# Optimization experiments

Measured on AMD Instinct MI355X. Metric: run time of the kernel, lower is better.

Reference implementation:

```python
import jax, jax.numpy as jnp
import numpy as np

N = 50000
E = 1600000
INPUT_DIM = 128
HEADS = 4
OUT_DIM = 32
LRELU_ALPHA = 0.2


def setup_inputs() -> dict:
    key = jax.random.key(0)
    k1, k2, k3, k4, k5 = jax.random.split(key, 5)
    gain = 1.0 / (1.0 + LRELU_ALPHA)
    input_proj = jax.random.normal(k1, (N, INPUT_DIM), dtype=jnp.float32)
    edge_index = jax.random.randint(k2, (2, E), 0, N, dtype=jnp.int64)
    W = jax.random.normal(k3, (INPUT_DIM, HEADS * OUT_DIM), dtype=jnp.float32) * (gain / INPUT_DIM) ** 0.5
    A_left = jax.random.normal(k4, (HEADS, OUT_DIM, 1), dtype=jnp.float32) * (gain / OUT_DIM)
    A_right = jax.random.normal(k5, (HEADS, OUT_DIM, 1), dtype=jnp.float32) * (gain / OUT_DIM)
    return {"input_proj": input_proj, "edge_index": edge_index, "W": W, "A_left": A_left, "A_right": A_right}


def reference(input_proj, edge_index, W, A_left, A_right):
    n = input_proj.shape[0]
    heads, out_dim = A_left.shape[0], A_left.shape[1]
    # Linear projection: [N, heads, out_dim]
    H = (input_proj @ W).reshape(n, heads, out_dim)
    # Per-node attention scores: [N, heads]
    H_s = jnp.einsum('nhd,hd->nh', H, A_left[..., 0])
    H_t = jnp.einsum('nhd,hd->nh', H, A_right[..., 0])
    src = edge_index[0]
    tgt = edge_index[1]
    # Edge scores: leaky_relu(H_s[src] + H_t[tgt]) -> [E, heads]
    e = H_s[src] + H_t[tgt]
    e = jnp.where(e > 0, e, LRELU_ALPHA * e)
    # Segment softmax over neighborhoods keyed by source node (global max shift, as in original)
    e = jnp.exp(e - jnp.max(e))
    denom = jax.ops.segment_sum(e, src, num_segments=n)  # [N, heads]
    alpha = e / (denom[src] + 1e-8)
    # Weighted scatter-add aggregation of target features: [N, heads, out_dim]
    msg = alpha[:, :, None] * H[tgt]
    agg = jax.ops.segment_sum(msg, src, num_segments=n)
    # concat_last=True -> [N, heads*out_dim], then ELU
    res = agg.reshape(n, heads * out_dim)
    return jax.nn.elu(res)
```

## Files before the change

kernel.cpp:

```cpp
#include <hip/hip_runtime.h>

#define DIM 128
#define HEADS 4
#define ODIM 32
#define LRELU 0.2f
#define PT 4096
#define CAP 9216

typedef unsigned int u32;
typedef unsigned short u16;
typedef unsigned char u8;

typedef __attribute__((ext_vector_type(8))) short bf16x8;
typedef __attribute__((ext_vector_type(4))) float f32x4;

__device__ __forceinline__ u16 f2bf(float f) {
    union { u32 u; float f; } x; x.f = f;
    u32 u = x.u;
    u32 r = u + 0x7FFFu + ((u >> 16) & 1u);
    return (u16)(r >> 16);
}
__device__ __forceinline__ float blo(u32 b) {
    union { u32 u; float f; } x; x.u = b << 16; return x.f;
}
__device__ __forceinline__ float bhi(u32 b) {
    union { u32 u; float f; } x; x.u = b & 0xFFFF0000u; return x.f;
}

__device__ __forceinline__ int scan256_excl(int v, int t, int* wsum) {
    int lane = t & 63, w = t >> 6;
    int inc = v;
    #pragma unroll
    for (int ofs = 1; ofs < 64; ofs <<= 1) {
        int x = __shfl_up(inc, ofs);
        if (lane >= ofs) inc += x;
    }
    __syncthreads();
    if (lane == 63) wsum[w] = inc;
    __syncthreads();
    int add = 0;
    #pragma unroll
    for (int j = 0; j < 4; ++j) add += (j < w) ? wsum[j] : 0;
    return inc - v + add;
}

__global__ __launch_bounds__(256) void prep_kernel(
    const float* __restrict__ W, u16* __restrict__ Wt, int* __restrict__ bcur)
{
    __shared__ u16 s[128 * 17];
    const int t = threadIdx.x;
    const int b = blockIdx.x;
    if (b == 0) bcur[t] = t * CAP;
    #pragma unroll
    for (int i = 0; i < 8; ++i) {
        int idx = i * 256 + t;
        int kk = idx >> 7;
        int nn = idx & 127;
        s[nn * 17 + kk] = f2bf(W[(b * 16 + kk) * 128 + nn]);
    }
    __syncthreads();
    #pragma unroll
    for (int i = 0; i < 8; ++i) {
        int idx = i * 256 + t;
        int nn = idx >> 4;
        int kk = idx & 15;
        Wt[nn * 128 + b * 16 + kk] = s[nn * 17 + kk];
    }
}

__device__ __forceinline__ void partition_body(
    char* smem, int bid, const int* __restrict__ ei, int* __restrict__ bcur,
    u32* __restrict__ part, int E, int n)
{
    u32* stage = (u32*)smem;
    u8*  sbkt  = (u8*)(smem + 16384);
    int (*lcnt4)[256] = (int (*)[256])(smem + 20480);
    int (*lcur4)[256] = (int (*)[256])(smem + 24576);
    int* loff  = (int*)(smem + 28672);
    int* ltot  = (int*)(smem + 29696);
    int* gbase = (int*)(smem + 30720);
    int* wsum  = (int*)(smem + 31744);
    const int t = threadIdx.x;
    const int wv = t >> 6;
    const int base = bid * PT;
    lcnt4[0][t] = 0; lcnt4[1][t] = 0; lcnt4[2][t] = 0; lcnt4[3][t] = 0;
    __syncthreads();

    u32 key[16];
    int bkt[16];
    #pragma unroll
    for (int i = 0; i < 16; ++i) {
        int e = base + i * 256 + t;
        bkt[i] = -1;
        key[i] = 0;
        if (e < E) {
            int src = ei[e];
            int tgt = ei[E + e];
            src = max(0, min(src, n - 1));
            tgt = max(0, min(tgt, n - 1));
            bkt[i] = src >> 8;
            key[i] = ((u32)(src & 255) << 17) | (u32)tgt;
            atomicAdd(&lcnt4[wv][bkt[i]], 1);
        }
    }
    __syncthreads();
    int c0 = lcnt4[0][t], c1 = lcnt4[1][t], c2 = lcnt4[2][t], c3 = lcnt4[3][t];
    int total = c0 + c1 + c2 + c3;
    int ex = scan256_excl(total, t, wsum);
    loff[t] = ex;
    ltot[t] = total;
    lcur4[0][t] = ex;
    lcur4[1][t] = ex + c0;
    lcur4[2][t] = ex + c0 + c1;
    lcur4[3][t] = ex + c0 + c1 + c2;
    gbase[t] = (total > 0) ? atomicAdd(&bcur[t], total) : 0;
    __syncthreads();
    #pragma unroll
    for (int i = 0; i < 16; ++i) {
        if (bkt[i] >= 0) {
            int p = atomicAdd(&lcur4[wv][bkt[i]], 1);
            stage[p] = key[i];
            sbkt[p] = (u8)bkt[i];
        }
    }
    __syncthreads();
    int tot = loff[255] + ltot[255];
    for (int i = t; i < tot; i += 256) {
        int b = sbkt[i];
        int dst = gbase[b] + (i - loff[b]);
        if (dst < (b + 1) * CAP) part[dst] = stage[i];
    }
}

__device__ __forceinline__ void proj_body(
    char* smem, int bid, const float* __restrict__ X, const u16* __restrict__ Wt,
    const float* __restrict__ AL, const float* __restrict__ AR,
    u32* __restrict__ Hb, float* __restrict__ Hs, float* __restrict__ Ht, int n)
{
    float* sH  = (float*)smem;
    float* sAL = (float*)(smem + 33792);
    float* sAR = (float*)(smem + 34304);
    const int t = threadIdx.x;
    if (t < DIM) { sAL[t] = AL[t]; sAR[t] = AR[t]; }
    const int row0 = bid * 64;
    const int w = t >> 6, lane = t & 63;
    const int quad = lane >> 4, nIdx = lane & 15;
    const int m = row0 + w * 16 + nIdx;

    f32x4 acc[8];
    #pragma unroll
    for (int c = 0; c < 8; ++c) acc[c] = (f32x4){0.f, 0.f, 0.f, 0.f};

    #pragma unroll
    for (int kq = 0; kq < 4; ++kq) {
        union { bf16x8 v; u16 e[8]; } a;
        if (m < n) {
            const float* xp = &X[(size_t)m * DIM + kq * 32 + quad * 8];
            float4 x0 = *(const float4*)xp;
            float4 x1 = *(const float4*)(xp + 4);
            a.e[0] = f2bf(x0.x); a.e[1] = f2bf(x0.y);
            a.e[2] = f2bf(x0.z); a.e[3] = f2bf(x0.w);
            a.e[4] = f2bf(x1.x); a.e[5] = f2bf(x1.y);
            a.e[6] = f2bf(x1.z); a.e[7] = f2bf(x1.w);
        } else {
            #pragma unroll
            for (int j = 0; j < 8; ++j) a.e[j] = 0;
        }
        #pragma unroll
        for (int c = 0; c < 8; ++c) {
            bf16x8 b = *(const bf16x8*)&Wt[(c * 16 + nIdx) * DIM + kq * 32 + quad * 8];
            acc[c] = __builtin_amdgcn_mfma_f32_16x16x32_bf16(a.v, b, acc[c], 0, 0, 0);
        }
    }
    #pragma unroll
    for (int c = 0; c < 8; ++c)
        #pragma unroll
        for (int r = 0; r < 4; ++r)
            sH[(w * 16 + quad * 4 + r) * 132 + c * 16 + nIdx] = acc[c][r];
    __syncthreads();

    #pragma unroll
    for (int i = 0; i < 16; ++i) {
        int idx = i * 256 + t;
        int r = idx >> 6, d2 = idx & 63;
        int gr = row0 + r;
        if (gr < n) {
            float2 hv = *(const float2*)&sH[r * 132 + 2 * d2];
            Hb[(size_t)gr * 64 + d2] = ((u32)f2bf(hv.y) << 16) | (u32)f2bf(hv.x);
        }
    }
    {
        int r = t >> 2, h = t & 3;
        float s = 0.f, s2 = 0.f;
        #pragma unroll
        for (int q = 0; q < ODIM; q += 4) {
            float4 hv = *(const float4*)&sH[r * 132 + h * ODIM + q];
            s  += hv.x*sAL[h*ODIM+q] + hv.y*sAL[h*ODIM+q+1] + hv.z*sAL[h*ODIM+q+2] + hv.w*sAL[h*ODIM+q+3];
            s2 += hv.x*sAR[h*ODIM+q] + hv.y*sAR[h*ODIM+q+1] + hv.z*sAR[h*ODIM+q+2] + hv.w*sAR[h*ODIM+q+3];
        }
        int gr = row0 + r;
        if (gr < n) { Hs[gr * HEADS + h] = s; Ht[gr * HEADS + h] = s2; }
    }
}

__global__ __launch_bounds__(256) void fused_pp_kernel(
    const float* __restrict__ X, const u16* __restrict__ Wt,
    const float* __restrict__ AL, const float* __restrict__ AR,
    u32* __restrict__ Hb, float* __restrict__ Hs, float* __restrict__ Ht,
    const int* __restrict__ ei, int* __restrict__ bcur, u32* __restrict__ part,
    int n, int E, int partBlocks)
{
    __shared__ alignas(16) char smem[34816];
    if ((int)blockIdx.x < partBlocks)
        partition_body(smem, blockIdx.x, ei, bcur, part, E, n);
    else
        proj_body(smem, blockIdx.x - partBlocks, X, Wt, AL, AR, Hb, Hs, Ht, n);
}

__global__ __launch_bounds__(256) void csrfill_kernel(
    const u32* __restrict__ part, const int* __restrict__ bcur,
    int* __restrict__ off, int* __restrict__ csr_tgt, int n, int ntiles)
{
    __shared__ int lc4[4][128];
    __shared__ int lcur4[4][128];
    __shared__ int wsum[4];
    __shared__ int sBase, sCnt;
    const int blk = blockIdx.x, t = threadIdx.x;
    const int b = blk >> 1, half = blk & 1;
    const int wv = t >> 6;
    int myc = (t < ntiles) ? (bcur[t] - t * CAP) : 0;
    myc = max(0, min(myc, CAP));
    int ex = scan256_excl(myc, t, wsum);
    if (t == b) { sBase = ex; sCnt = myc; }
    if (t < 128) { lc4[0][t] = 0; lc4[1][t] = 0; lc4[2][t] = 0; lc4[3][t] = 0; }
    __syncthreads();
    const int pbase = b * CAP;
    const int base = sBase, cnt = sCnt;
    for (int i = t; i < cnt; i += 256) {
        int node8 = part[pbase + i] >> 17;
        if ((node8 >> 7) == half) atomicAdd(&lc4[wv][node8 & 127], 1);
    }
    __syncthreads();
    int c0 = 0, c1 = 0, c2 = 0, c3 = 0, total = 0;
    if (t < 128) {
        c0 = lc4[0][t]; c1 = lc4[1][t]; c2 = lc4[2][t]; c3 = lc4[3][t];
        total = c0 + c1 + c2 + c3;
    }
    int ex2 = scan256_excl(total, t, wsum);
    int halfTot = wsum[0] + wsum[1];
    int myBase = base + (half ? (cnt - halfTot) : 0);
    if (t < 128) {
        lcur4[0][t] = ex2;
        lcur4[1][t] = ex2 + c0;
        lcur4[2][t] = ex2 + c0 + c1;
        lcur4[3][t] = ex2 + c0 + c1 + c2;
        int node = b * 256 + half * 128 + t;
        if (node < n) off[node] = myBase + ex2;
    }
    if (b == ntiles - 1 && half == 0 && t == 0) off[n] = base + cnt;
    __syncthreads();
    for (int i = t; i < cnt; i += 256) {
        u32 key = part[pbase + i];
        int node8 = key >> 17;
        if ((node8 >> 7) == half) {
            int p = atomicAdd(&lcur4[wv][node8 & 127], 1);
            csr_tgt[myBase + p] = (int)(key & 0x1FFFFu);
        }
    }
}

__global__ __launch_bounds__(256) void agg_kernel(
    const u32* __restrict__ Hb, const float* __restrict__ Hs,
    const float* __restrict__ Ht, const int* __restrict__ off,
    const int* __restrict__ csr_tgt, float2* __restrict__ out, int n, int E)
{
    int node = (blockIdx.x * 256 + threadIdx.x) >> 6;
    int L = threadIdx.x & 63;
    if (node >= n) return;
    int lo = off[node], hi = off[node + 1];
    lo = max(0, min(lo, E));
    hi = max(lo, min(hi, E));
    const int h = L >> 4;
    const int eSel = (L & 31) >> 2;
    const int hSel = L & 3;
    float4 hs4 = *(const float4*)&Hs[node * HEADS];
    float hsC = hSel == 0 ? hs4.x : hSel == 1 ? hs4.y : hSel == 2 ? hs4.z : hs4.w;
    float hsO = h == 0 ? hs4.x : h == 1 ? hs4.y : h == 2 ? hs4.z : hs4.w;
    float ax = 0.f, ay = 0.f, Sd = 0.f, Srem = 0.f;

    int i = lo;
    for (; i + 8 <= hi; i += 8) {
        int tt[8];
        #pragma unroll
        for (int j = 0; j < 8; ++j) tt[j] = csr_tgt[i + j];
        int tsel = csr_tgt[i + eSel];
        float e = hsC + Ht[tsel * HEADS + hSel];
        float w = __expf(fminf(e > 0.f ? e : LRELU * e, 30.f));
        Sd += w;
        u32 bb[8];
        #pragma unroll
        for (int j = 0; j < 8; ++j) bb[j] = Hb[tt[j] * 64 + L];
        #pragma unroll
        for (int j = 0; j < 8; ++j) {
            float wj = __shfl(w, (j << 2) | h);
            ax += wj * blo(bb[j]);
            ay += wj * bhi(bb[j]);
        }
    }
    for (; i < hi; ++i) {
        int tgt = csr_tgt[i];
        float e = hsO + Ht[tgt * HEADS + h];
        float w = __expf(fminf(e > 0.f ? e : LRELU * e, 30.f));
        u32 b = Hb[tgt * 64 + L];
        ax += w * blo(b);
        ay += w * bhi(b);
        Srem += w;
    }
    float S = Srem;
    #pragma unroll
    for (int j = 0; j < 8; ++j) S += __shfl(Sd, (j << 2) | h);
    float inv = 1.f / (S + 1e-8f);
    float ox = ax * inv, oy = ay * inv;
    ox = ox > 0.f ? ox : (__expf(ox) - 1.f);
    oy = oy > 0.f ? oy : (__expf(oy) - 1.f);
    out[(size_t)node * 64 + L] = {ox, oy};
}

extern "C" void kernel_launch(void* const* d_in, const int* in_sizes, int n_in,
                              void* d_out, int out_size, void* d_ws, size_t ws_size,
                              hipStream_t stream) {
    const float* X  = (const float*)d_in[0];
    const int*   EI = (const int*)d_in[1];
    const float* W  = (const float*)d_in[2];
    const float* AL = (const float*)d_in[3];
    const float* AR = (const float*)d_in[4];
    const int n = in_sizes[0] / DIM;
    const int E = in_sizes[1] / 2;
    const int ntiles = (n + 255) / 256;

    char* ws = (char*)d_ws;
    size_t o = 0;
    auto alloc = [&](size_t bytes) -> void* {
        o = (o + 255) & ~(size_t)255;
        void* p = ws + o;
        o += bytes;
        return p;
    };
    int*   bcur    = (int*)alloc(256 * 4);
    u16*   Wt      = (u16*)alloc((size_t)DIM * DIM * 2);
    int*   off     = (int*)alloc((size_t)(n + 1) * 4);
    float* Hs      = (float*)alloc((size_t)n * HEADS * 4);
    float* Ht      = (float*)alloc((size_t)n * HEADS * 4);
    int*   csr_tgt = (int*)alloc((size_t)E * 4);
    u32*   part    = (u32*)alloc((size_t)ntiles * CAP * 4);
    u32*   Hb      = (u32*)alloc((size_t)n * 64 * 4);

    const int PB = (E + PT - 1) / PT;
    const int JB = (n + 63) / 64;

    prep_kernel<<<8, 256, 0, stream>>>(W, Wt, bcur);
    fused_pp_kernel<<<PB + JB, 256, 0, stream>>>(
        X, Wt, AL, AR, Hb, Hs, Ht, EI, bcur, part, n, E, PB);
    csrfill_kernel<<<ntiles * 2, 256, 0, stream>>>(part, bcur, off, csr_tgt, n, ntiles);
    agg_kernel<<<(n + 3) / 4, 256, 0, stream>>>(
        Hb, Hs, Ht, off, csr_tgt, (float2*)d_out, n, E);
}
```

Baseline: 194.3 us.

## Batch loads for more memory parallelism in partition, CSR and aggregation kernels

The partition kernel now issues all 16 source loads and then all 16 target loads before computing keys and doing the shared atomics, so the loads can overlap. The CSR build loops are unrolled four ways, with the loads grouped ahead of the atomics. The aggregation kernel processes 16 edges per step using all 64 lanes for the attention weights, and masks the tail edges instead of running a scalar remainder loop. Nodes with no edges exit early and write zero. In exchange, register pressure rises, and nodes with few edges (the average degree is about 32) do padded work that is masked off.

```diff
diff --git a/kernel.cpp b/kernel.cpp
--- a/kernel.cpp
+++ b/kernel.cpp
@@ -86,23 +86,33 @@
     lcnt4[0][t] = 0; lcnt4[1][t] = 0; lcnt4[2][t] = 0; lcnt4[3][t] = 0;
     __syncthreads();
 
+    int srcv[16], tgtv[16];
+    #pragma unroll
+    for (int i = 0; i < 16; ++i) {
+        int e = base + i * 256 + t;
+        srcv[i] = (e < E) ? ei[e] : -1;
+    }
+    #pragma unroll
+    for (int i = 0; i < 16; ++i) {
+        int e = base + i * 256 + t;
+        tgtv[i] = (e < E) ? ei[E + e] : 0;
+    }
     u32 key[16];
     int bkt[16];
     #pragma unroll
     for (int i = 0; i < 16; ++i) {
-        int e = base + i * 256 + t;
         bkt[i] = -1;
         key[i] = 0;
-        if (e < E) {
-            int src = ei[e];
-            int tgt = ei[E + e];
-            src = max(0, min(src, n - 1));
-            tgt = max(0, min(tgt, n - 1));
+        if (srcv[i] >= 0) {
+            int src = min(srcv[i], n - 1);
+            int tgt = max(0, min(tgtv[i], n - 1));
             bkt[i] = src >> 8;
             key[i] = ((u32)(src & 255) << 17) | (u32)tgt;
-            atomicAdd(&lcnt4[wv][bkt[i]], 1);
-        }
-    }
+        }
+    }
+    #pragma unroll
+    for (int i = 0; i < 16; ++i)
+        if (bkt[i] >= 0) atomicAdd(&lcnt4[wv][bkt[i]], 1);
     __syncthreads();
     int c0 = lcnt4[0][t], c1 = lcnt4[1][t], c2 = lcnt4[2][t], c3 = lcnt4[3][t];
     int total = c0 + c1 + c2 + c3;
@@ -236,9 +246,18 @@
     __syncthreads();
     const int pbase = b * CAP;
     const int base = sBase, cnt = sCnt;
-    for (int i = t; i < cnt; i += 256) {
-        int node8 = part[pbase + i] >> 17;
-        if ((node8 >> 7) == half) atomicAdd(&lc4[wv][node8 & 127], 1);
+    for (int i = t; i < cnt; i += 1024) {
+        u32 k[4];
+        #pragma unroll
+        for (int u = 0; u < 4; ++u) {
+            int idx = i + u * 256;
+            k[u] = (idx < cnt) ? part[pbase + idx] : 0xFFFFFFFFu;
+        }
+        #pragma unroll
+        for (int u = 0; u < 4; ++u) {
+            int n8 = (int)(k[u] >> 17);
+            if ((n8 >> 7) == half) atomicAdd(&lc4[wv][n8 & 127], 1);
+        }
     }
     __syncthreads();
     int c0 = 0, c1 = 0, c2 = 0, c3 = 0, total = 0;
@@ -259,12 +278,20 @@
     }
     if (b == ntiles - 1 && half == 0 && t == 0) off[n] = base + cnt;
     __syncthreads();
-    for (int i = t; i < cnt; i += 256) {
-        u32 key = part[pbase + i];
-        int node8 = key >> 17;
-        if ((node8 >> 7) == half) {
-            int p = atomicAdd(&lcur4[wv][node8 & 127], 1);
-            csr_tgt[myBase + p] = (int)(key & 0x1FFFFu);
+    for (int i = t; i < cnt; i += 1024) {
+        u32 k[4];
+        #pragma unroll
+        for (int u = 0; u < 4; ++u) {
+            int idx = i + u * 256;
+            k[u] = (idx < cnt) ? part[pbase + idx] : 0xFFFFFFFFu;
+        }
+        #pragma unroll
+        for (int u = 0; u < 4; ++u) {
+            int n8 = (int)(k[u] >> 17);
+            if ((n8 >> 7) == half) {
+                int p = atomicAdd(&lcur4[wv][n8 & 127], 1);
+                csr_tgt[myBase + p] = (int)(k[u] & 0x1FFFFu);
+            }
         }
     }
 }
@@ -280,45 +307,40 @@
     int lo = off[node], hi = off[node + 1];
     lo = max(0, min(lo, E));
     hi = max(lo, min(hi, E));
+    if (hi <= lo) {
+        out[(size_t)node * 64 + L] = {0.f, 0.f};
+        return;
+    }
     const int h = L >> 4;
-    const int eSel = (L & 31) >> 2;
+    const int jSel = L >> 2;
     const int hSel = L & 3;
     float4 hs4 = *(const float4*)&Hs[node * HEADS];
-    float hsC = hSel == 0 ? hs4.x : hSel == 1 ? hs4.y : hSel == 2 ? hs4.z : hs4.w;
-    float hsO = h == 0 ? hs4.x : h == 1 ? hs4.y : h == 2 ? hs4.z : hs4.w;
-    float ax = 0.f, ay = 0.f, Sd = 0.f, Srem = 0.f;
-
-    int i = lo;
-    for (; i + 8 <= hi; i += 8) {
-        int tt[8];
-        #pragma unroll
-        for (int j = 0; j < 8; ++j) tt[j] = csr_tgt[i + j];
-        int tsel = csr_tgt[i + eSel];
-        float e = hsC + Ht[tsel * HEADS + hSel];
-        float w = __expf(fminf(e > 0.f ? e : LRELU * e, 30.f));
+    float hsD = hSel == 0 ? hs4.x : hSel == 1 ? hs4.y : hSel == 2 ? hs4.z : hs4.w;
+    float ax = 0.f, ay = 0.f, Sd = 0.f;
+
+    for (int i = lo; i < hi; i += 16) {
+        int tt[16];
+        #pragma unroll
+        for (int j = 0; j < 16; ++j) tt[j] = csr_tgt[min(i + j, hi - 1)];
+        int tsel = csr_tgt[min(i + jSel, hi - 1)];
+        float e = hsD + Ht[tsel * HEADS + hSel];
+        float w = (i + jSel < hi)
+                      ? __expf(fminf(e > 0.f ? e : LRELU * e, 30.f))
+                      : 0.f;
         Sd += w;
-        u32 bb[8];
-        #pragma unroll
-        for (int j = 0; j < 8; ++j) bb[j] = Hb[tt[j] * 64 + L];
-        #pragma unroll
-        for (int j = 0; j < 8; ++j) {
+        u32 bb[16];
+        #pragma unroll
+        for (int j = 0; j < 16; ++j) bb[j] = Hb[tt[j] * 64 + L];
+        #pragma unroll
+        for (int j = 0; j < 16; ++j) {
             float wj = __shfl(w, (j << 2) | h);
             ax += wj * blo(bb[j]);
             ay += wj * bhi(bb[j]);
         }
     }
-    for (; i < hi; ++i) {
-        int tgt = csr_tgt[i];
-        float e = hsO + Ht[tgt * HEADS + h];
-        float w = __expf(fminf(e > 0.f ? e : LRELU * e, 30.f));
-        u32 b = Hb[tgt * 64 + L];
-        ax += w * blo(b);
-        ay += w * bhi(b);
-        Srem += w;
-    }
-    float S = Srem;
-    #pragma unroll
-    for (int j = 0; j < 8; ++j) S += __shfl(Sd, (j << 2) | h);
+    float S = 0.f;
+    #pragma unroll
+    for (int j = 0; j < 16; ++j) S += __shfl(Sd, (j << 2) | h);
     float inv = 1.f / (S + 1e-8f);
     float ox = ax * inv, oy = ay * inv;
     ox = ox > 0.f ? ox : (__expf(ox) - 1.f);
```

After: 188.1 us. 1.03x faster.
